# Optimization experiments

Measured on AMD Instinct MI355X. Metric: run time of the kernel, lower is better.

## Reference

```python
import jax, jax.numpy as jnp
import numpy as np

STRIDE = 2
PAD = 1
K = 4
OUT_PAD = 0


def setup_inputs() -> dict:
    key = jax.random.key(0)
    k1, k2, k3, k4 = jax.random.split(key, 4)
    x = jax.random.normal(k1, (16, 64, 128, 128), dtype=jnp.float32)
    # torch ConvTranspose2d weight layout: [in_channels, out_channels, kH, kW]
    w = jax.random.normal(k2, (64, 32, 4, 4), dtype=jnp.float32) * 0.05
    conv_b = jax.random.normal(k3, (32,), dtype=jnp.float32) * 0.05
    bias = jax.random.normal(k4, (1, 1, 1, 1), dtype=jnp.float32)
    return {"x": x, "w": w, "conv_b": conv_b, "bias": bias}


def conv_transpose2d(x, w, conv_b):
    # Equivalent of torch ConvTranspose2d(k=4, s=2, p=1, op=0):
    # dilate input by stride, pad by k-1-p (+op on trailing side), conv with flipped kernel.
    lo = K - 1 - PAD
    hi = K - 1 - PAD + OUT_PAD
    w_oihw = jnp.flip(w, axis=(2, 3)).transpose(1, 0, 2, 3)  # [Cout, Cin, kH, kW]
    y = jax.lax.conv_general_dilated(
        x, w_oihw,
        window_strides=(1, 1),
        padding=((lo, hi), (lo, hi)),
        lhs_dilation=(STRIDE, STRIDE),
        dimension_numbers=("NCHW", "OIHW", "NCHW"),
    )
    return y + conv_b[None, :, None, None]


def reference(x, w, conv_b, bias):
    y = conv_transpose2d(x, w, conv_b)          # [N, Cout, H', W']
    y = jnp.min(y, axis=1, keepdims=True)       # channel-min -> [N,1,H',W']
    y = jnp.sum(y, axis=2, keepdims=True)       # height-sum  -> [N,1,1,W']
    # kernel uses tanh-based GELU approximation
    return jax.nn.gelu(y, approximate=True) + bias
```

## Files before the change

### kernel.cpp

```cpp
#include <hip/hip_runtime.h>
#include <math.h>

typedef __attribute__((ext_vector_type(8))) short short8;
typedef __attribute__((ext_vector_type(16))) float f32x16;

#define XS_STRIDE 72

__device__ __forceinline__ short f2bf(float f) {
    union { float f; unsigned u; } v; v.f = f;
    unsigned r = (v.u + 0x7FFFu + ((v.u >> 16) & 1u)) >> 16;
    return (short)r;
}

__global__ void zero_acc(float* __restrict__ acc) {
    acc[blockIdx.x * 256 + threadIdx.x] = 0.f;
}

__global__ void build_wfrag(const float* __restrict__ w, short* __restrict__ wfrag) {
    int idx = blockIdx.x * 256 + threadIdx.x;
    int j    = idx & 7;
    int lane = (idx >> 3) & 63;
    int q    = (idx >> 9) & 15;
    int p    = idx >> 13;
    int co = lane & 31, half = lane >> 5;
    int ci = (q & 3) * 16 + half * 8 + j;
    int t = q >> 2, a = t >> 1, b = t & 1;
    int ph = p >> 1, pw = p & 1;
    int kh = 2 * a + 1 - ph, kw = 2 * b + 1 - pw;
    wfrag[idx] = f2bf(w[((ci * 32 + co) * 4 + kh) * 4 + kw]);
}

__global__ __launch_bounds__(256, 4) void convt_mfma(
    const float* __restrict__ x, const short* __restrict__ wfrag,
    const float* __restrict__ conv_b, float* __restrict__ acc4096)
{
    __shared__ short xs[4][66][XS_STRIDE];
    __shared__ float minbuf[2][4][64];

    int blk = blockIdx.x;
    int jh = blk & 1;
    int i0 = ((blk >> 1) & 63) * 2;
    int n  = blk >> 7;
    int t  = threadIdx.x;

    {
        int col  = t & 63;
        int cih  = (t >> 6) * 4;
        int gcol = jh * 64 + col;
        for (int r = 0; r < 4; ++r) {
            int gi = i0 - 1 + r;
            bool rowok = (unsigned)gi < 128u;
            int gic = rowok ? gi : 0;
            for (int g = 0; g < 4; ++g) {
                int ci = g * 16 + cih;
                const float* px = x + (((size_t)(n * 64 + ci) * 128 + gic) * 128 + gcol);
                float v0 = rowok ? px[0]     : 0.f;
                float v1 = rowok ? px[16384] : 0.f;
                float v2 = rowok ? px[32768] : 0.f;
                float v3 = rowok ? px[49152] : 0.f;
                union { short s[4]; unsigned long long u; } pk;
                pk.s[0] = f2bf(v0); pk.s[1] = f2bf(v1);
                pk.s[2] = f2bf(v2); pk.s[3] = f2bf(v3);
                *(unsigned long long*)&xs[r][col + 1][ci] = pk.u;
            }
        }
        {
            int r = t >> 6, ci = t & 63, gi = i0 - 1 + r;
            for (int side = 0; side < 2; ++side) {
                int gc = jh * 64 + (side ? 64 : -1);
                float v = ((unsigned)gi < 128u && (unsigned)gc < 128u)
                        ? x[((size_t)(n * 64 + ci) * 128 + gi) * 128 + gc] : 0.f;
                xs[r][side ? 65 : 0][ci] = f2bf(v);
            }
        }
    }
    __syncthreads();

    int wv = t >> 6, lane = t & 63;
    int ph = wv >> 1, pw = wv & 1;
    int ln = lane & 31, half = lane >> 5;

    short8 af[16];
    const short8* wf = (const short8*)(wfrag + wv * 8192);
    #pragma unroll
    for (int q = 0; q < 16; ++q) af[q] = wf[q * 64 + lane];

    float cb[16];
    #pragma unroll
    for (int reg = 0; reg < 16; ++reg) {
        int co = (reg & 3) + 8 * (reg >> 2) + 4 * half;
        cb[reg] = conv_b[co];
    }

    #pragma unroll
    for (int rp = 0; rp < 2; ++rp) {
        for (int j0 = 0; j0 < 64; j0 += 32) {
            f32x16 acc;
            #pragma unroll
            for (int reg = 0; reg < 16; ++reg) acc[reg] = cb[reg];
            #pragma unroll
            for (int q = 0; q < 16; ++q) {
                int tq = q >> 2, a = tq >> 1, b = tq & 1;
                int ridx = rp + 1 + ph - a;
                int colp = j0 + ln + (pw - b) + 1;
                int ci0  = (q & 3) * 16 + half * 8;
                const short8* bp = (const short8*)&xs[ridx][colp][ci0];
                acc = __builtin_amdgcn_mfma_f32_32x32x16_bf16(af[q], *bp, acc, 0, 0, 0);
            }
            float mn = acc[0];
            #pragma unroll
            for (int reg = 1; reg < 16; ++reg) mn = fminf(mn, acc[reg]);
            mn = fminf(mn, __shfl_xor(mn, 32, 64));
            if (half == 0) minbuf[rp][wv][j0 + ln] = mn;
        }
    }
    __syncthreads();

    {
        int rp  = t >> 7;
        int pw2 = (t >> 6) & 1;
        int jl  = t & 63;
        float v = minbuf[rp][pw2][jl] + minbuf[rp][2 + pw2][jl];
        int ow = ((jh * 64 + jl) << 1) | pw2;
        atomicAdd(&acc4096[n * 256 + ow], v);
    }
}

__global__ void finalize(const float* __restrict__ acc4096,
                         const float* __restrict__ bias, float* __restrict__ out)
{
    int idx = blockIdx.x * 256 + threadIdx.x;
    float s = acc4096[idx];
    float u = 0.7978845608028654f * (s + 0.044715f * s * s * s);
    out[idx] = 0.5f * s * (1.f + tanhf(u)) + bias[0];
}

extern "C" void kernel_launch(void* const* d_in, const int* in_sizes, int n_in,
                              void* d_out, int out_size, void* d_ws, size_t ws_size,
                              hipStream_t stream) {
    const float* x      = (const float*)d_in[0];
    const float* w      = (const float*)d_in[1];
    const float* conv_b = (const float*)d_in[2];
    const float* bias   = (const float*)d_in[3];
    float* out = (float*)d_out;

    float* acc   = (float*)d_ws;
    short* wfrag = (short*)((char*)d_ws + 16384);

    hipLaunchKernelGGL(zero_acc, dim3(16), dim3(256), 0, stream, acc);
    hipLaunchKernelGGL(build_wfrag, dim3(128), dim3(256), 0, stream, w, wfrag);
    hipLaunchKernelGGL(convt_mfma, dim3(16 * 64 * 2), dim3(256), 0, stream,
                       x, wfrag, conv_b, acc);
    hipLaunchKernelGGL(finalize, dim3(16), dim3(256), 0, stream,
                       acc, bias, out);
}
```

Baseline: 136.4 us.

## Stream input rows through LDS ring buffer with register prefetch per block

```diff
diff --git a/kernel.cpp b/kernel.cpp
--- a/kernel.cpp
+++ b/kernel.cpp
@@ -3,8 +3,10 @@
 
 typedef __attribute__((ext_vector_type(8))) short short8;
 typedef __attribute__((ext_vector_type(16))) float f32x16;
+typedef __attribute__((ext_vector_type(2))) unsigned uintx2;
 
 #define XS_STRIDE 72
+#define RING 6
 
 __device__ __forceinline__ short f2bf(float f) {
     union { float f; unsigned u; } v; v.f = f;
@@ -12,116 +14,194 @@
     return (short)r;
 }
 
-__global__ void zero_acc(float* __restrict__ acc) {
-    acc[blockIdx.x * 256 + threadIdx.x] = 0.f;
-}
-
-__global__ void build_wfrag(const float* __restrict__ w, short* __restrict__ wfrag) {
+__device__ __forceinline__ unsigned cvt_pk_bf16(float lo, float hi) {
+    unsigned r;
+    asm("v_cvt_pk_bf16_f32 %0, %1, %2" : "=v"(r) : "v"(lo), "v"(hi));
+    return r;
+}
+
+__global__ void prep(const float* __restrict__ w, short* __restrict__ wfrag,
+                     float* __restrict__ acc) {
+    if (blockIdx.x >= 128) {
+        #pragma unroll
+        for (int i = 0; i < 16; ++i) acc[i * 256 + threadIdx.x] = 0.f;
+        return;
+    }
     int idx = blockIdx.x * 256 + threadIdx.x;
     int j    = idx & 7;
     int lane = (idx >> 3) & 63;
     int q    = (idx >> 9) & 15;
     int p    = idx >> 13;
-    int co = lane & 31, half = lane >> 5;
-    int ci = (q & 3) * 16 + half * 8 + j;
-    int t = q >> 2, a = t >> 1, b = t & 1;
+    int co = lane & 31, hf = lane >> 5;
+    int ci = (q & 3) * 16 + hf * 8 + j;
+    int tq = q >> 2, a = tq >> 1, b = tq & 1;
     int ph = p >> 1, pw = p & 1;
     int kh = 2 * a + 1 - ph, kw = 2 * b + 1 - pw;
     wfrag[idx] = f2bf(w[((ci * 32 + co) * 4 + kh) * 4 + kw]);
 }
 
-__global__ __launch_bounds__(256, 4) void convt_mfma(
+__global__ __launch_bounds__(256, 3) void convt_mfma(
     const float* __restrict__ x, const short* __restrict__ wfrag,
     const float* __restrict__ conv_b, float* __restrict__ acc4096)
 {
-    __shared__ short xs[4][66][XS_STRIDE];
-    __shared__ float minbuf[2][4][64];
-
-    int blk = blockIdx.x;
-    int jh = blk & 1;
-    int i0 = ((blk >> 1) & 63) * 2;
-    int n  = blk >> 7;
-    int t  = threadIdx.x;
-
+    __shared__ short xs[RING][34][XS_STRIDE];
+    __shared__ float minbuf[2][2][4][32];
+
+    const int blk = blockIdx.x;
+    const int jq = blk & 3;
+    const int st = (blk >> 2) & 15;
+    const int n  = blk >> 6;
+    const int t  = threadIdx.x;
+    const int i0 = st * 8;
+
+    const int wv = t >> 6, lane = t & 63;
+    const int ph = wv >> 1, pw = wv & 1;
+    const int ln = lane & 31, half = lane >> 5;
+
+    short8 af[16];
     {
-        int col  = t & 63;
-        int cih  = (t >> 6) * 4;
-        int gcol = jh * 64 + col;
-        for (int r = 0; r < 4; ++r) {
-            int gi = i0 - 1 + r;
+        const short8* wf = (const short8*)(wfrag + wv * 8192);
+        #pragma unroll
+        for (int q = 0; q < 16; ++q) af[q] = wf[q * 64 + lane];
+    }
+    float cb[16];
+    #pragma unroll
+    for (int reg = 0; reg < 16; ++reg)
+        cb[reg] = conv_b[(reg & 3) + 8 * (reg >> 2) + 4 * half];
+
+    const float* xn = x + (size_t)n * 64 * 128 * 128;
+
+    const int col  = t & 31;
+    const int cib  = (t >> 5) * 8;
+    const int gcol = jq * 32 + col;
+    const int hrow = t >> 7, hside = (t >> 6) & 1, hci = t & 63;
+    const int hgc  = jq * 32 + (hside ? 32 : -1);
+    const int sl_base = i0 % RING;
+
+    #pragma unroll
+    for (int r = 0; r < 4; ++r) {
+        int gi = i0 - 1 + r;
+        int slot = sl_base + r; if (slot >= RING) slot -= RING;
+        bool rowok = (unsigned)gi < 128u;
+        int gic = rowok ? gi : 0;
+        const float* px = xn + ((size_t)cib * 128 + gic) * 128 + gcol;
+        float v[8];
+        #pragma unroll
+        for (int c = 0; c < 8; ++c) v[c] = rowok ? px[c * 16384] : 0.f;
+        uintx2 u0, u1;
+        u0.x = cvt_pk_bf16(v[0], v[1]); u0.y = cvt_pk_bf16(v[2], v[3]);
+        u1.x = cvt_pk_bf16(v[4], v[5]); u1.y = cvt_pk_bf16(v[6], v[7]);
+        *(uintx2*)&xs[slot][col + 1][cib]     = u0;
+        *(uintx2*)&xs[slot][col + 1][cib + 4] = u1;
+    }
+    {
+        int r = t >> 6, ci = t & 63, gi = i0 - 1 + r;
+        int slot = sl_base + r; if (slot >= RING) slot -= RING;
+        #pragma unroll
+        for (int side = 0; side < 2; ++side) {
+            int gc = jq * 32 + (side ? 32 : -1);
+            float v = ((unsigned)gi < 128u && (unsigned)gc < 128u)
+                    ? xn[((size_t)ci * 128 + gi) * 128 + gc] : 0.f;
+            xs[slot][side ? 33 : 0][ci] = f2bf(v);
+        }
+    }
+
+    float pf[2][8]; float pfh;
+    auto issue = [&](int r0) {
+        #pragma unroll
+        for (int r2 = 0; r2 < 2; ++r2) {
+            int gi = r0 + r2;
             bool rowok = (unsigned)gi < 128u;
             int gic = rowok ? gi : 0;
-            for (int g = 0; g < 4; ++g) {
-                int ci = g * 16 + cih;
-                const float* px = x + (((size_t)(n * 64 + ci) * 128 + gic) * 128 + gcol);
-                float v0 = rowok ? px[0]     : 0.f;
-                float v1 = rowok ? px[16384] : 0.f;
-                float v2 = rowok ? px[32768] : 0.f;
-                float v3 = rowok ? px[49152] : 0.f;
-                union { short s[4]; unsigned long long u; } pk;
-                pk.s[0] = f2bf(v0); pk.s[1] = f2bf(v1);
-                pk.s[2] = f2bf(v2); pk.s[3] = f2bf(v3);
-                *(unsigned long long*)&xs[r][col + 1][ci] = pk.u;
+            const float* px = xn + ((size_t)cib * 128 + gic) * 128 + gcol;
+            #pragma unroll
+            for (int c = 0; c < 8; ++c) pf[r2][c] = rowok ? px[c * 16384] : 0.f;
+        }
+        int gi = r0 + hrow;
+        pfh = ((unsigned)gi < 128u && (unsigned)hgc < 128u)
+            ? xn[((size_t)hci * 128 + gi) * 128 + hgc] : 0.f;
+    };
+    issue(i0 + 3);
+
+    __syncthreads();
+
+    float osum = 0.f;
+    const int rpr = t >> 6;
+    const int pw2 = (t >> 5) & 1;
+    const int jl  = t & 31;
+
+    int rbase = sl_base;
+    #pragma unroll
+    for (int k = 0; k < 4; ++k) {
+        const int kb = k & 1;
+        int s0 = rbase + ph; if (s0 >= RING) s0 -= RING;
+        int s1 = s0 + 1;     if (s1 >= RING) s1 -= RING;
+        int s2 = s1 + 1;     if (s2 >= RING) s2 -= RING;
+
+        f32x16 acc0, acc1;
+        #pragma unroll
+        for (int reg = 0; reg < 16; ++reg) { acc0[reg] = cb[reg]; acc1[reg] = cb[reg]; }
+        __builtin_amdgcn_s_setprio(1);
+        #pragma unroll
+        for (int b = 0; b < 2; ++b) {
+            int colp = ln + (pw - b) + 1;
+            const short* p0 = &xs[s0][colp][half * 8];
+            const short* p1 = &xs[s1][colp][half * 8];
+            const short* p2 = &xs[s2][colp][half * 8];
+            #pragma unroll
+            for (int c = 0; c < 4; ++c) {
+                short8 Fs = *(const short8*)(p1 + c * 16);
+                acc0 = __builtin_amdgcn_mfma_f32_32x32x16_bf16(af[4*b+c],   Fs, acc0, 0, 0, 0);
+                acc1 = __builtin_amdgcn_mfma_f32_32x32x16_bf16(af[8+4*b+c], Fs, acc1, 0, 0, 0);
+                short8 F0 = *(const short8*)(p0 + c * 16);
+                acc0 = __builtin_amdgcn_mfma_f32_32x32x16_bf16(af[8+4*b+c], F0, acc0, 0, 0, 0);
+                short8 F2 = *(const short8*)(p2 + c * 16);
+                acc1 = __builtin_amdgcn_mfma_f32_32x32x16_bf16(af[4*b+c],   F2, acc1, 0, 0, 0);
             }
         }
-        {
-            int r = t >> 6, ci = t & 63, gi = i0 - 1 + r;
-            for (int side = 0; side < 2; ++side) {
-                int gc = jh * 64 + (side ? 64 : -1);
-                float v = ((unsigned)gi < 128u && (unsigned)gc < 128u)
-                        ? x[((size_t)(n * 64 + ci) * 128 + gi) * 128 + gc] : 0.f;
-                xs[r][side ? 65 : 0][ci] = f2bf(v);
+        __builtin_amdgcn_s_setprio(0);
+
+        float mn0 = acc0[0], mn1 = acc1[0];
+        #pragma unroll
+        for (int reg = 1; reg < 16; ++reg) {
+            mn0 = fminf(mn0, acc0[reg]); mn1 = fminf(mn1, acc1[reg]);
+        }
+        mn0 = fminf(mn0, __shfl_xor(mn0, 32, 64));
+        mn1 = fminf(mn1, __shfl_xor(mn1, 32, 64));
+        if (half == 0) {
+            minbuf[kb][0][wv][ln] = mn0;
+            minbuf[kb][1][wv][ln] = mn1;
+        }
+
+        if (k < 3) {
+            int ws0 = rbase + 4; if (ws0 >= RING) ws0 -= RING;
+            int ws1 = ws0 + 1;   if (ws1 >= RING) ws1 -= RING;
+            #pragma unroll
+            for (int r2 = 0; r2 < 2; ++r2) {
+                int slot = r2 ? ws1 : ws0;
+                uintx2 u0, u1;
+                u0.x = cvt_pk_bf16(pf[r2][0], pf[r2][1]);
+                u0.y = cvt_pk_bf16(pf[r2][2], pf[r2][3]);
+                u1.x = cvt_pk_bf16(pf[r2][4], pf[r2][5]);
+                u1.y = cvt_pk_bf16(pf[r2][6], pf[r2][7]);
+                *(uintx2*)&xs[slot][col + 1][cib]     = u0;
+                *(uintx2*)&xs[slot][col + 1][cib + 4] = u1;
             }
-        }
-    }
+            xs[hrow ? ws1 : ws0][hside ? 33 : 0][hci] = f2bf(pfh);
+            if (k < 2) issue(i0 + 2 * k + 5);
+        }
+        __syncthreads();
+        if (t < 128)
+            osum += minbuf[kb][rpr][pw2][jl] + minbuf[kb][rpr][2 + pw2][jl];
+        rbase += 2; if (rbase >= RING) rbase -= RING;
+    }
+
+    float* sbuf = &minbuf[0][0][0][0];
+    if (t < 128) sbuf[t] = osum;
     __syncthreads();
-
-    int wv = t >> 6, lane = t & 63;
-    int ph = wv >> 1, pw = wv & 1;
-    int ln = lane & 31, half = lane >> 5;
-
-    short8 af[16];
-    const short8* wf = (const short8*)(wfrag + wv * 8192);
-    #pragma unroll
-    for (int q = 0; q < 16; ++q) af[q] = wf[q * 64 + lane];
-
-    float cb[16];
-    #pragma unroll
-    for (int reg = 0; reg < 16; ++reg) {
-        int co = (reg & 3) + 8 * (reg >> 2) + 4 * half;
-        cb[reg] = conv_b[co];
-    }
-
-    #pragma unroll
-    for (int rp = 0; rp < 2; ++rp) {
-        for (int j0 = 0; j0 < 64; j0 += 32) {
-            f32x16 acc;
-            #pragma unroll
-            for (int reg = 0; reg < 16; ++reg) acc[reg] = cb[reg];
-            #pragma unroll
-            for (int q = 0; q < 16; ++q) {
-                int tq = q >> 2, a = tq >> 1, b = tq & 1;
-                int ridx = rp + 1 + ph - a;
-                int colp = j0 + ln + (pw - b) + 1;
-                int ci0  = (q & 3) * 16 + half * 8;
-                const short8* bp = (const short8*)&xs[ridx][colp][ci0];
-                acc = __builtin_amdgcn_mfma_f32_32x32x16_bf16(af[q], *bp, acc, 0, 0, 0);
-            }
-            float mn = acc[0];
-            #pragma unroll
-            for (int reg = 1; reg < 16; ++reg) mn = fminf(mn, acc[reg]);
-            mn = fminf(mn, __shfl_xor(mn, 32, 64));
-            if (half == 0) minbuf[rp][wv][j0 + ln] = mn;
-        }
-    }
-    __syncthreads();
-
-    {
-        int rp  = t >> 7;
-        int pw2 = (t >> 6) & 1;
-        int jl  = t & 63;
-        float v = minbuf[rp][pw2][jl] + minbuf[rp][2 + pw2][jl];
-        int ow = ((jh * 64 + jl) << 1) | pw2;
+    if (t < 64) {
+        float v = sbuf[t] + sbuf[t + 64];
+        int ow = ((jq * 32 + (t & 31)) << 1) | ((t >> 5) & 1);
         atomicAdd(&acc4096[n * 256 + ow], v);
     }
 }
@@ -147,9 +227,8 @@
     float* acc   = (float*)d_ws;
     short* wfrag = (short*)((char*)d_ws + 16384);
 
-    hipLaunchKernelGGL(zero_acc, dim3(16), dim3(256), 0, stream, acc);
-    hipLaunchKernelGGL(build_wfrag, dim3(128), dim3(256), 0, stream, w, wfrag);
-    hipLaunchKernelGGL(convt_mfma, dim3(16 * 64 * 2), dim3(256), 0, stream,
+    hipLaunchKernelGGL(prep, dim3(129), dim3(256), 0, stream, w, wfrag, acc);
+    hipLaunchKernelGGL(convt_mfma, dim3(16 * 16 * 4), dim3(256), 0, stream,
                        x, wfrag, conv_b, acc);
     hipLaunchKernelGGL(finalize, dim3(16), dim3(256), 0, stream,
                        acc, bias, out);
```

Measured after the change: 123.8 us. 9.2% less time.
